# Kernel tuning notes

Hardware: AMD Instinct MI355X
Metric: run time of the kernel (lower is better)

Reference implementation:

```python
import jax, jax.numpy as jnp
import numpy as np

B, S, N = 1, 256, 384
MSA_S, Z_D = 64, 128
H, C_H = 8, 32
C_OPM = 32
INF = 1e9

def ln(x, w, b):
    mu = jnp.mean(x, -1, keepdims=True)
    var = jnp.mean(jnp.square(x - mu), -1, keepdims=True)
    return (x - mu) * jax.lax.rsqrt(var + 1e-5) * w + b

def setup_inputs() -> dict:
    key = jax.random.key(0)
    ks = jax.random.split(key, 16)
    def lin(k, out_d, in_d):
        return jax.random.normal(k, (out_d, in_d), jnp.float32) / np.sqrt(in_d)
    return {
        "z": jax.random.normal(ks[0], (B, N, N, Z_D), jnp.float32),
        "m": jax.random.normal(ks[1], (B, S, N, MSA_S), jnp.float32),
        "token_mask": jnp.ones((B, N, N), jnp.float32),
        "msa_mask": jnp.ones((B, S, N), jnp.float32),
        "norm_z_w": jnp.ones((Z_D,), jnp.float32), "norm_z_b": jnp.zeros((Z_D,), jnp.float32),
        "proj_z_w": lin(ks[2], H, Z_D),
        "norm_m_w": jnp.ones((MSA_S,), jnp.float32), "norm_m_b": jnp.zeros((MSA_S,), jnp.float32),
        "proj_m_w": lin(ks[3], H * C_H, MSA_S),
        "proj_g_w": lin(ks[4], H * C_H, MSA_S),
        "pwa_proj_o_w": lin(ks[5], MSA_S, H * C_H),
        "trans_norm_w": jnp.ones((MSA_S,), jnp.float32), "trans_norm_b": jnp.zeros((MSA_S,), jnp.float32),
        "fc1_w": lin(ks[6], 4 * MSA_S, MSA_S),
        "fc2_w": lin(ks[7], 4 * MSA_S, MSA_S),
        "fc3_w": lin(ks[8], MSA_S, 4 * MSA_S),
        "opm_norm_w": jnp.ones((MSA_S,), jnp.float32), "opm_norm_b": jnp.zeros((MSA_S,), jnp.float32),
        "proj_a_w": lin(ks[9], C_OPM, MSA_S),
        "proj_b_w": lin(ks[10], C_OPM, MSA_S),
        "opm_proj_o_w": lin(ks[11], Z_D, C_OPM * C_OPM),
        "opm_proj_o_b": jnp.zeros((Z_D,), jnp.float32),
    }

def reference(z, m, token_mask, msa_mask,
              norm_z_w, norm_z_b, proj_z_w,
              norm_m_w, norm_m_b, proj_m_w, proj_g_w, pwa_proj_o_w,
              trans_norm_w, trans_norm_b, fc1_w, fc2_w, fc3_w,
              opm_norm_w, opm_norm_b, proj_a_w, proj_b_w, opm_proj_o_w, opm_proj_o_b):
    # --- PairWeightedAveraging: pair-biased, gated MSA row attention ---
    b_full = ln(z, norm_z_w, norm_z_b) @ proj_z_w.T                     # [B,N,N,H]
    bias = jnp.transpose(b_full, (0, 3, 1, 2)) + (1.0 - token_mask[:, None]) * (-INF)
    w = jax.nn.softmax(bias, axis=-1)                                   # [B,H,N,N]
    mn = ln(m, norm_m_w, norm_m_b)
    v = (mn @ proj_m_w.T).reshape(B, S, N, H, C_H)                      # [B,S,N,H,c]
    g = jax.nn.sigmoid(mn @ proj_g_w.T)                                 # [B,S,N,H*c]
    o = jnp.einsum('bhij,bsjhd->bsihd', w, v).reshape(B, S, N, H * C_H)
    m = m + (g * o) @ pwa_proj_o_w.T
    # --- MSA transition (SwiGLU) ---
    tn = ln(m, trans_norm_w, trans_norm_b)
    m = m + (jax.nn.silu(tn @ fc1_w.T) * (tn @ fc2_w.T)) @ fc3_w.T
    # --- OuterProductMean -> pair update ---
    mk = msa_mask[..., None]                                            # [B,S,N,1]
    on = ln(m, opm_norm_w, opm_norm_b)
    a = (on @ proj_a_w.T) * mk                                          # [B,S,N,c]
    bb = (on @ proj_b_w.T) * mk                                         # [B,S,N,c]
    num_mask = jnp.clip(jnp.einsum('bsi,bsj->bij', msa_mask, msa_mask), 1.0, None)[..., None]
    opm = jnp.einsum('bsic,bsjd->bijcd', a, bb).reshape(B, N, N, C_OPM * C_OPM) / num_mask
    z = z + opm @ opm_proj_o_w.T + opm_proj_o_b
    return (z, m)
```

## Files before the change

### kernel.cpp

```cpp
#include <hip/hip_runtime.h>
#include <math.h>

constexpr int NRES = 384;
constexpr int NSEQ = 256;
constexpr int DM   = 64;
constexpr int DZ   = 128;
constexpr int NH   = 8;
constexpr int DH   = 32;
constexpr int HC   = NH * DH;
constexpr int DOP  = 32;
constexpr int FF   = 4 * DM;

constexpr int NPAIR = NRES * NRES;
constexpr int NROWS = NSEQ * NRES;
constexpr int ZTOT  = NPAIR * DZ;
constexpr int SD    = NSEQ * DH;

typedef unsigned short ushort_t;
typedef __attribute__((ext_vector_type(8))) short short8;
typedef __attribute__((ext_vector_type(4))) short short4_t;
typedef __attribute__((ext_vector_type(4))) float f32x4;

__device__ __forceinline__ float wred_sum(float v) {
    #pragma unroll
    for (int off = 32; off; off >>= 1) v += __shfl_xor(v, off, 64);
    return v;
}
__device__ __forceinline__ float sigm(float x) { return 1.0f / (1.0f + expf(-x)); }
__device__ __forceinline__ ushort_t cvt_bf(float f) {
    unsigned u = __float_as_uint(f);
    unsigned r = (u + 0x7FFFu + ((u >> 16) & 1u)) >> 16;
    return (ushort_t)r;
}
__device__ __forceinline__ float cvt_f(ushort_t h) {
    return __uint_as_float(((unsigned)h) << 16);
}
__device__ __forceinline__ f32x4 mfma16(short8 a, short8 b, f32x4 c) {
    return __builtin_amdgcn_mfma_f32_16x16x32_bf16(a, b, c, 0, 0, 0);
}
__device__ __forceinline__ void gld16(const ushort_t* g, ushort_t* l) {
    __builtin_amdgcn_global_load_lds(
        (const __attribute__((address_space(1))) unsigned int*)g,
        (__attribute__((address_space(3))) unsigned int*)l, 16, 0, 0);
}

__global__ __launch_bounds__(256) void k_prep(const float* __restrict__ f1,
                                              const float* __restrict__ f2,
                                              const float* __restrict__ f3,
                                              const float* __restrict__ opW,
                                              const float* __restrict__ pmw,
                                              const float* __restrict__ pgw,
                                              const float* __restrict__ pow_,
                                              const float* __restrict__ paw,
                                              const float* __restrict__ pbw,
                                              const float* __restrict__ pzw,
                                              ushort_t* __restrict__ f1b,
                                              ushort_t* __restrict__ f2b,
                                              ushort_t* __restrict__ f3b,
                                              ushort_t* __restrict__ opWb,
                                              ushort_t* __restrict__ pmwb,
                                              ushort_t* __restrict__ pgwb,
                                              ushort_t* __restrict__ powb,
                                              ushort_t* __restrict__ abwb,
                                              ushort_t* __restrict__ pzwb) {
    int i = blockIdx.x * 256 + threadIdx.x;
    opWb[i] = cvt_bf(opW[i]);
    if (i < FF * DM) {
        f1b[i] = cvt_bf(f1[i]);
        f2b[i] = cvt_bf(f2[i]);
        f3b[i] = cvt_bf(f3[i]);
    }
    if (i < HC * DM) {
        pmwb[i] = cvt_bf(pmw[i]);
        pgwb[i] = cvt_bf(pgw[i]);
        powb[i] = cvt_bf(pow_[i]);
    }
    if (i < 2 * DOP * DM) {
        abwb[i] = cvt_bf(i < DOP * DM ? paw[i] : pbw[i - DOP * DM]);
    }
    if (i < 16 * DZ) {
        pzwb[i] = (i < NH * DZ) ? cvt_bf(pzw[i]) : (ushort_t)0;
    }
}

__global__ __launch_bounds__(256) void k_biassm(const float* __restrict__ z,
                                                const float* __restrict__ nzw,
                                                const float* __restrict__ nzb,
                                                const ushort_t* __restrict__ pzwb,
                                                const float* __restrict__ tmask,
                                                ushort_t* __restrict__ wsb) {
    int i = blockIdx.x;
    __shared__ ushort_t Azl[128][136];
    __shared__ ushort_t Bl[16][136];
    __shared__ float ob[8][388];
    __shared__ float wln[128], bln[128];
    int t = threadIdx.x;
    if (t < 128) { wln[t] = nzw[t]; bln[t] = nzb[t]; }
    int wave = t >> 6, lane = t & 63;
    int lk = (lane >> 4) * 8, lr = lane & 15;
    int wr = wave * 32;
    for (int idx = t * 8; idx < 16 * DZ; idx += 256 * 8) {
        int row = idx >> 7, col = idx & 127;
        *(short8*)&Bl[row][col] = *(const short8*)&pzwb[idx];
    }
    __syncthreads();
    for (int c = 0; c < 3; c++) {
        {
            int jl = t >> 1, cb = (t & 1) * 64;
            const float* src = &z[((size_t)i * NRES + c * 128 + jl) * DZ + cb];
            float4 v[16];
            float s1 = 0.0f, s2 = 0.0f;
            #pragma unroll
            for (int q = 0; q < 16; q++) {
                v[q] = *(const float4*)&src[q * 4];
                s1 += v[q].x + v[q].y + v[q].z + v[q].w;
                s2 += v[q].x * v[q].x + v[q].y * v[q].y + v[q].z * v[q].z + v[q].w * v[q].w;
            }
            s1 += __shfl_xor(s1, 1, 64);
            s2 += __shfl_xor(s2, 1, 64);
            float mu = s1 * (1.0f / 128.0f);
            float var = s2 * (1.0f / 128.0f) - mu * mu;
            float rs = rsqrtf(var + 1e-5f);
            #pragma unroll
            for (int q = 0; q < 8; q++) {
                float4 xa = v[2 * q], xb = v[2 * q + 1];
                int base = cb + q * 8;
                short8 o;
                o[0] = (short)cvt_bf((xa.x - mu) * rs * wln[base + 0] + bln[base + 0]);
                o[1] = (short)cvt_bf((xa.y - mu) * rs * wln[base + 1] + bln[base + 1]);
                o[2] = (short)cvt_bf((xa.z - mu) * rs * wln[base + 2] + bln[base + 2]);
                o[3] = (short)cvt_bf((xa.w - mu) * rs * wln[base + 3] + bln[base + 3]);
                o[4] = (short)cvt_bf((xb.x - mu) * rs * wln[base + 4] + bln[base + 4]);
                o[5] = (short)cvt_bf((xb.y - mu) * rs * wln[base + 5] + bln[base + 5]);
                o[6] = (short)cvt_bf((xb.z - mu) * rs * wln[base + 6] + bln[base + 6]);
                o[7] = (short)cvt_bf((xb.w - mu) * rs * wln[base + 7] + bln[base + 7]);
                *(short8*)&Azl[jl][base] = o;
            }
        }
        __syncthreads();
        f32x4 acc[2] = {};
        #pragma unroll
        for (int ks = 0; ks < 4; ks++) {
            short8 b = *(const short8*)&Bl[lr][ks * 32 + lk];
            short8 a0 = *(const short8*)&Azl[wr + lr][ks * 32 + lk];
            short8 a1 = *(const short8*)&Azl[wr + 16 + lr][ks * 32 + lk];
            acc[0] = mfma16(a0, b, acc[0]);
            acc[1] = mfma16(a1, b, acc[1]);
        }
        if (lr < NH) {
            #pragma unroll
            for (int ri = 0; ri < 2; ri++) {
                int jb = c * 128 + wr + 16 * ri + (lane >> 4) * 4;
                #pragma unroll
                for (int r = 0; r < 4; r++)
                    ob[lr][jb + r] = acc[ri][r];
            }
        }
        __syncthreads();
    }
    int h = wave * 2 + (lane >> 5);
    int l32 = lane & 31;
    int jb = l32 * 12;
    const float* tm = &tmask[(size_t)i * NRES];
    float vals[12];
    float mx = -1e30f;
    #pragma unroll
    for (int q = 0; q < 12; q++) {
        float v = ob[h][jb + q] + (1.0f - tm[jb + q]) * (-1e9f);
        vals[q] = v;
        mx = fmaxf(mx, v);
    }
    #pragma unroll
    for (int off = 16; off; off >>= 1) mx = fmaxf(mx, __shfl_xor(mx, off, 64));
    float sum = 0.0f;
    #pragma unroll
    for (int q = 0; q < 12; q++) { vals[q] = expf(vals[q] - mx); sum += vals[q]; }
    #pragma unroll
    for (int off = 16; off; off >>= 1) sum += __shfl_xor(sum, off, 64);
    float inv = 1.0f / sum;
    ushort_t* o = &wsb[(size_t)h * NPAIR + (size_t)i * NRES + jb];
    #pragma unroll
    for (int q = 0; q < 12; q++) o[q] = cvt_bf(vals[q] * inv);
}

__global__ __launch_bounds__(256) void k_ln64(const float* __restrict__ src,
                                              const float* __restrict__ lw,
                                              const float* __restrict__ lb,
                                              ushort_t* __restrict__ dst) {
    int wave = threadIdx.x >> 6, lane = threadIdx.x & 63;
    int r = blockIdx.x * 4 + wave;
    float x = src[(size_t)r * DM + lane];
    float mu = wred_sum(x) * (1.0f / 64.0f);
    float d = x - mu;
    float var = wred_sum(d * d) * (1.0f / 64.0f);
    dst[(size_t)r * DM + lane] = cvt_bf(d * rsqrtf(var + 1e-5f) * lw[lane] + lb[lane]);
}

__global__ __launch_bounds__(256) void k_vproj_mfma(const ushort_t* __restrict__ A,
                                                    const ushort_t* __restrict__ Bt,
                                                    ushort_t* __restrict__ vtt) {
    int m0 = blockIdx.y * 64, n0c = blockIdx.x * 64;
    __shared__ ushort_t Al[64][40];
    __shared__ ushort_t Bl[64][40];
    __shared__ ushort_t ot[64][72];
    int t = threadIdx.x;
    int srow = t >> 2, sko = (t & 3) * 8;
    int wave = t >> 6, lane = t & 63;
    int wr = (wave >> 1) * 32, wc = (wave & 1) * 32;
    int lk = (lane >> 4) * 8, lr = lane & 15;
    f32x4 acc[2][2] = {};
    for (int k0 = 0; k0 < DM; k0 += 32) {
        *(short8*)&Al[srow][sko] = *(const short8*)&A[(size_t)(m0 + srow) * DM + k0 + sko];
        *(short8*)&Bl[srow][sko] = *(const short8*)&Bt[(size_t)(n0c + srow) * DM + k0 + sko];
        __syncthreads();
        short8 a0 = *(const short8*)&Al[wr + lr][lk];
        short8 a1 = *(const short8*)&Al[wr + 16 + lr][lk];
        short8 b0 = *(const short8*)&Bl[wc + lr][lk];
        short8 b1 = *(const short8*)&Bl[wc + 16 + lr][lk];
        acc[0][0] = mfma16(a0, b0, acc[0][0]);
        acc[0][1] = mfma16(a0, b1, acc[0][1]);
        acc[1][0] = mfma16(a1, b0, acc[1][0]);
        acc[1][1] = mfma16(a1, b1, acc[1][1]);
        __syncthreads();
    }
    #pragma unroll
    for (int ri = 0; ri < 2; ri++)
        #pragma unroll
        for (int ci = 0; ci < 2; ci++) {
            int rowb = wr + 16 * ri + (lane >> 4) * 4;
            int colb = wc + 16 * ci + lr;
            #pragma unroll
            for (int r = 0; r < 4; r++)
                ot[colb][rowb + r] = cvt_bf(acc[ri][ci][r]);
        }
    __syncthreads();
    int s = m0 / NRES, n0 = m0 % NRES;
    int h0 = n0c >> 5;
    int orow = t >> 2, seg = (t & 3) * 16;
    short8 v0 = *(const short8*)&ot[orow][seg];
    short8 v1 = *(const short8*)&ot[orow][seg + 8];
    int hh = orow >> 5, dd = orow & 31;
    ushort_t* dst = &vtt[(((size_t)(h0 + hh) * SD) + s * DH + dd) * NRES + n0 + seg];
    *(short8*)&dst[0] = v0;
    *(short8*)&dst[8] = v1;
}

__global__ __launch_bounds__(256) void k_tr(const ushort_t* __restrict__ src,
                                            ushort_t* __restrict__ dst,
                                            int R, int C) {
    size_t bs = (size_t)R * C;
    const ushort_t* s = src + blockIdx.z * bs;
    ushort_t* d = dst + blockIdx.z * bs;
    int r0 = blockIdx.y * 64, c0 = blockIdx.x * 64;
    __shared__ ushort_t tile[64][72];
    int t = threadIdx.x;
    int tr = t >> 2, tc = (t & 3) * 16;
    *(short8*)&tile[tr][tc]     = *(const short8*)&s[(size_t)(r0 + tr) * C + c0 + tc];
    *(short8*)&tile[tr][tc + 8] = *(const short8*)&s[(size_t)(r0 + tr) * C + c0 + tc + 8];
    __syncthreads();
    short8 o0, o1;
    #pragma unroll
    for (int i = 0; i < 8; i++) {
        o0[i] = (short)tile[tc + i][tr];
        o1[i] = (short)tile[tc + 8 + i][tr];
    }
    *(short8*)&d[(size_t)(c0 + tr) * R + r0 + tc]     = o0;
    *(short8*)&d[(size_t)(c0 + tr) * R + r0 + tc + 8] = o1;
}

__global__ __launch_bounds__(256) void k_attn_mfma(const ushort_t* __restrict__ wsb,
                                                   const ushort_t* __restrict__ vtt,
                                                   ushort_t* __restrict__ otb2) {
    int h = blockIdx.z;
    const ushort_t* A  = wsb + (size_t)h * NPAIR;
    const ushort_t* Bt = vtt + (size_t)h * SD * NRES;
    int m0 = blockIdx.y * 128, n0 = blockIdx.x * 128;
    __shared__ ushort_t Al[128 * 32];
    __shared__ ushort_t Bl[128 * 32];
    int t = threadIdx.x;
    int w = t >> 6, lane = t & 63;
    int wr = (w >> 1) * 64, wc = (w & 1) * 64;
    int lq = lane >> 4, lr = lane & 15;
    int rS = w * 16 + (lane >> 2);
    int cqs = (((lane & 3) ^ ((rS >> 1) & 3)) << 3);
    f32x4 acc[4][4] = {};
    for (int k0 = 0; k0 < NRES; k0 += 32) {
        gld16(&A [(size_t)(m0 + rS)      * NRES + k0 + cqs], &Al[(w * 16) * 32]);
        gld16(&A [(size_t)(m0 + 64 + rS) * NRES + k0 + cqs], &Al[(64 + w * 16) * 32]);
        gld16(&Bt[(size_t)(n0 + rS)      * NRES + k0 + cqs], &Bl[(w * 16) * 32]);
        gld16(&Bt[(size_t)(n0 + 64 + rS) * NRES + k0 + cqs], &Bl[(64 + w * 16) * 32]);
        __syncthreads();
        short8 af[4], bf2[4];
        #pragma unroll
        for (int i = 0; i < 4; i++) {
            int ra = wr + 16 * i + lr;
            int rb = wc + 16 * i + lr;
            af[i]  = *(const short8*)&Al[ra * 32 + ((lq ^ ((ra >> 1) & 3)) << 3)];
            bf2[i] = *(const short8*)&Bl[rb * 32 + ((lq ^ ((rb >> 1) & 3)) << 3)];
        }
        #pragma unroll
        for (int ri = 0; ri < 4; ri++)
            #pragma unroll
            for (int ci = 0; ci < 4; ci++)
                acc[ri][ci] = mfma16(af[ri], bf2[ci], acc[ri][ci]);
        __syncthreads();
    }
    #pragma unroll
    for (int ri = 0; ri < 4; ri++)
        #pragma unroll
        for (int ci = 0; ci < 4; ci++) {
            int row0 = m0 + wr + 16 * ri + (lane >> 4) * 4;
            int col  = n0 + wc + 16 * ci + lr;
            int s = col >> 5, dd = col & 31;
            #pragma unroll
            for (int r = 0; r < 4; r++)
                otb2[((size_t)s * NRES + row0 + r) * HC + h * DH + dd] = cvt_bf(acc[ri][ci][r]);
        }
}

__global__ __launch_bounds__(256) void k_gateout(const ushort_t* __restrict__ A,
                                                 const ushort_t* __restrict__ Bg,
                                                 const ushort_t* __restrict__ otb2,
                                                 const ushort_t* __restrict__ Bo,
                                                 const float* __restrict__ m,
                                                 float* __restrict__ mout,
                                                 const float* __restrict__ tnw,
                                                 const float* __restrict__ tnb,
                                                 ushort_t* __restrict__ tn_bf) {
    int m0 = blockIdx.x * 64;
    __shared__ ushort_t Al[64][72];
    __shared__ ushort_t Bl[64][72];
    __shared__ ushort_t go[64][264];
    int t = threadIdx.x;
    int srow = t >> 2, sko = (t & 3) * 16;
    int wave = t >> 6, lane = t & 63;
    int wr = (wave >> 1) * 32, wc = (wave & 1) * 32;
    int lk = (lane >> 4) * 8, lr = lane & 15;
    float tw = tnw[lane], tb = tnb[lane];
    {
        const ushort_t* arow = &A[(size_t)(m0 + srow) * DM + sko];
        *(short8*)&Al[srow][sko]     = *(const short8*)&arow[0];
        *(short8*)&Al[srow][sko + 8] = *(const short8*)&arow[8];
    }
    __syncthreads();
    short8 a[2][2];
    a[0][0] = *(const short8*)&Al[wr + lr][lk];
    a[0][1] = *(const short8*)&Al[wr + lr][32 + lk];
    a[1][0] = *(const short8*)&Al[wr + 16 + lr][lk];
    a[1][1] = *(const short8*)&Al[wr + 16 + lr][32 + lk];
    for (int nq = 0; nq < 4; nq++) {
        __syncthreads();
        {
            const ushort_t* brow = &Bg[(size_t)(nq * 64 + srow) * DM + sko];
            *(short8*)&Bl[srow][sko]     = *(const short8*)&brow[0];
            *(short8*)&Bl[srow][sko + 8] = *(const short8*)&brow[8];
        }
        __syncthreads();
        f32x4 acc[2][2] = {};
        #pragma unroll
        for (int ks = 0; ks < 2; ks++) {
            short8 b0 = *(const short8*)&Bl[wc + lr][ks * 32 + lk];
            short8 b1 = *(const short8*)&Bl[wc + 16 + lr][ks * 32 + lk];
            acc[0][0] = mfma16(a[0][ks], b0, acc[0][0]);
            acc[0][1] = mfma16(a[0][ks], b1, acc[0][1]);
            acc[1][0] = mfma16(a[1][ks], b0, acc[1][0]);
            acc[1][1] = mfma16(a[1][ks], b1, acc[1][1]);
        }
        #pragma unroll
        for (int ri = 0; ri < 2; ri++)
            #pragma unroll
            for (int ci = 0; ci < 2; ci++) {
                int lrow = wr + 16 * ri + (lane >> 4) * 4;
                int col  = nq * 64 + wc + 16 * ci + lr;
                #pragma unroll
                for (int r = 0; r < 4; r++) {
                    float ov = cvt_f(otb2[(size_t)(m0 + lrow + r) * HC + col]);
                    go[lrow + r][col] = cvt_bf(sigm(acc[ri][ci][r]) * ov);
                }
            }
    }
    f32x4 acc[2][2] = {};
    for (int k0 = 0; k0 < HC; k0 += 32) {
        __syncthreads();
        *(short8*)&Bl[t >> 2][(t & 3) * 8] = *(const short8*)&Bo[(size_t)(t >> 2) * HC + k0 + (t & 3) * 8];
        __syncthreads();
        short8 a0 = *(const short8*)&go[wr + lr][k0 + lk];
        short8 a1 = *(const short8*)&go[wr + 16 + lr][k0 + lk];
        short8 b0 = *(const short8*)&Bl[wc + lr][lk];
        short8 b1 = *(const short8*)&Bl[wc + 16 + lr][lk];
        acc[0][0] = mfma16(a0, b0, acc[0][0]);
        acc[0][1] = mfma16(a0, b1, acc[0][1]);
        acc[1][0] = mfma16(a1, b0, acc[1][0]);
        acc[1][1] = mfma16(a1, b1, acc[1][1]);
    }
    __syncthreads();
    #pragma unroll
    for (int ri = 0; ri < 2; ri++)
        #pragma unroll
        for (int ci = 0; ci < 2; ci++) {
            int lrow0 = wr + 16 * ri + (lane >> 4) * 4;
            int col   = wc + 16 * ci + lr;
            #pragma unroll
            for (int r = 0; r < 4; r++) {
                size_t idx = (size_t)(m0 + lrow0 + r) * DM + col;
                float v = m[idx] + acc[ri][ci][r];
                mout[idx] = v;
                go[lrow0 + r][col] = cvt_bf(v);
            }
        }
    __syncthreads();
    for (int rr = 0; rr < 16; rr++) {
        int row = wave * 16 + rr;
        float x = cvt_f(go[row][lane]);
        float mu = wred_sum(x) * (1.0f / 64.0f);
        float d = x - mu;
        float var = wred_sum(d * d) * (1.0f / 64.0f);
        tn_bf[(size_t)(m0 + row) * DM + lane] = cvt_bf(d * rsqrtf(var + 1e-5f) * tw + tb);
    }
}

__global__ __launch_bounds__(256) void k_fctrans(const ushort_t* __restrict__ A,
                                                 const ushort_t* __restrict__ B1,
                                                 const ushort_t* __restrict__ B2,
                                                 const ushort_t* __restrict__ B3,
                                                 float* __restrict__ mio,
                                                 const float* __restrict__ onw,
                                                 const float* __restrict__ onb,
                                                 ushort_t* __restrict__ onb_bf) {
    int m0 = blockIdx.x * 64;
    __shared__ ushort_t Al[64][72];
    __shared__ ushort_t B1l[64][72];
    __shared__ ushort_t B2l[64][72];
    __shared__ ushort_t hhl[64][264];
    int t = threadIdx.x;
    int srow = t >> 2, sko = (t & 3) * 16;
    int wave = t >> 6, lane = t & 63;
    int wr = (wave >> 1) * 32, wc = (wave & 1) * 32;
    int lk = (lane >> 4) * 8, lr = lane & 15;
    float ow = onw[lane], ob = onb[lane];
    {
        const ushort_t* arow = &A[(size_t)(m0 + srow) * DM + sko];
        *(short8*)&Al[srow][sko]     = *(const short8*)&arow[0];
        *(short8*)&Al[srow][sko + 8] = *(const short8*)&arow[8];
    }
    __syncthreads();
    short8 a[2][2];
    a[0][0] = *(const short8*)&Al[wr + lr][lk];
    a[0][1] = *(const short8*)&Al[wr + lr][32 + lk];
    a[1][0] = *(const short8*)&Al[wr + 16 + lr][lk];
    a[1][1] = *(const short8*)&Al[wr + 16 + lr][32 + lk];
    for (int nq = 0; nq < 4; nq++) {
        __syncthreads();
        {
            const ushort_t* b1r = &B1[(size_t)(nq * 64 + srow) * DM + sko];
            const ushort_t* b2r = &B2[(size_t)(nq * 64 + srow) * DM + sko];
            *(short8*)&B1l[srow][sko]     = *(const short8*)&b1r[0];
            *(short8*)&B1l[srow][sko + 8] = *(const short8*)&b1r[8];
            *(short8*)&B2l[srow][sko]     = *(const short8*)&b2r[0];
            *(short8*)&B2l[srow][sko + 8] = *(const short8*)&b2r[8];
        }
        __syncthreads();
        f32x4 acc1[2][2] = {}, acc2[2][2] = {};
        #pragma unroll
        for (int ks = 0; ks < 2; ks++) {
            short8 p0 = *(const short8*)&B1l[wc + lr][ks * 32 + lk];
            short8 p1 = *(const short8*)&B1l[wc + 16 + lr][ks * 32 + lk];
            short8 q0 = *(const short8*)&B2l[wc + lr][ks * 32 + lk];
            short8 q1 = *(const short8*)&B2l[wc + 16 + lr][ks * 32 + lk];
            acc1[0][0] = mfma16(a[0][ks], p0, acc1[0][0]);
            acc1[0][1] = mfma16(a[0][ks], p1, acc1[0][1]);
            acc1[1][0] = mfma16(a[1][ks], p0, acc1[1][0]);
            acc1[1][1] = mfma16(a[1][ks], p1, acc1[1][1]);
            acc2[0][0] = mfma16(a[0][ks], q0, acc2[0][0]);
            acc2[0][1] = mfma16(a[0][ks], q1, acc2[0][1]);
            acc2[1][0] = mfma16(a[1][ks], q0, acc2[1][0]);
            acc2[1][1] = mfma16(a[1][ks], q1, acc2[1][1]);
        }
        #pragma unroll
        for (int ri = 0; ri < 2; ri++)
            #pragma unroll
            for (int ci = 0; ci < 2; ci++) {
                int lrow = wr + 16 * ri + (lane >> 4) * 4;
                int col  = nq * 64 + wc + 16 * ci + lr;
                #pragma unroll
                for (int r = 0; r < 4; r++) {
                    float a1v = acc1[ri][ci][r], a2v = acc2[ri][ci][r];
                    hhl[lrow + r][col] = cvt_bf(a1v * sigm(a1v) * a2v);
                }
            }
    }
    f32x4 acc[2][2] = {};
    for (int k0 = 0; k0 < FF; k0 += 32) {
        __syncthreads();
        *(short8*)&B1l[t >> 2][(t & 3) * 8] = *(const short8*)&B3[(size_t)(t >> 2) * FF + k0 + (t & 3) * 8];
        __syncthreads();
        short8 a0 = *(const short8*)&hhl[wr + lr][k0 + lk];
        short8 a1 = *(const short8*)&hhl[wr + 16 + lr][k0 + lk];
        short8 b0 = *(const short8*)&B1l[wc + lr][lk];
        short8 b1 = *(const short8*)&B1l[wc + 16 + lr][lk];
        acc[0][0] = mfma16(a0, b0, acc[0][0]);
        acc[0][1] = mfma16(a0, b1, acc[0][1]);
        acc[1][0] = mfma16(a1, b0, acc[1][0]);
        acc[1][1] = mfma16(a1, b1, acc[1][1]);
    }
    __syncthreads();
    #pragma unroll
    for (int ri = 0; ri < 2; ri++)
        #pragma unroll
        for (int ci = 0; ci < 2; ci++) {
            int lrow0 = wr + 16 * ri + (lane >> 4) * 4;
            int col   = wc + 16 * ci + lr;
            #pragma unroll
            for (int r = 0; r < 4; r++) {
                size_t idx = (size_t)(m0 + lrow0 + r) * DM + col;
                float v = mio[idx] + acc[ri][ci][r];
                mio[idx] = v;
                hhl[lrow0 + r][col] = cvt_bf(v);
            }
        }
    __syncthreads();
    for (int rr = 0; rr < 16; rr++) {
        int row = wave * 16 + rr;
        float x = cvt_f(hhl[row][lane]);
        float mu = wred_sum(x) * (1.0f / 64.0f);
        float d = x - mu;
        float var = wred_sum(d * d) * (1.0f / 64.0f);
        onb_bf[(size_t)(m0 + row) * DM + lane] = cvt_bf(d * rsqrtf(var + 1e-5f) * ow + ob);
    }
}

__global__ __launch_bounds__(256) void k_ab_mfma(const ushort_t* __restrict__ A,
                                                 const ushort_t* __restrict__ Bt,
                                                 const float* __restrict__ smask,
                                                 ushort_t* __restrict__ abuf,
                                                 ushort_t* __restrict__ bbuf) {
    int m0 = blockIdx.x * 64;
    __shared__ ushort_t Al[64][40];
    __shared__ ushort_t Bl[64][40];
    int t = threadIdx.x;
    int srow = t >> 2, sko = (t & 3) * 8;
    int wave = t >> 6, lane = t & 63;
    int wr = (wave >> 1) * 32, wc = (wave & 1) * 32;
    int lk = (lane >> 4) * 8, lr = lane & 15;
    f32x4 acc[2][2] = {};
    for (int k0 = 0; k0 < DM; k0 += 32) {
        *(short8*)&Al[srow][sko] = *(const short8*)&A[(size_t)(m0 + srow) * DM + k0 + sko];
        *(short8*)&Bl[srow][sko] = *(const short8*)&Bt[(size_t)srow * DM + k0 + sko];
        __syncthreads();
        short8 a0 = *(const short8*)&Al[wr + lr][lk];
        short8 a1 = *(const short8*)&Al[wr + 16 + lr][lk];
        short8 b0 = *(const short8*)&Bl[wc + lr][lk];
        short8 b1 = *(const short8*)&Bl[wc + 16 + lr][lk];
        acc[0][0] = mfma16(a0, b0, acc[0][0]);
        acc[0][1] = mfma16(a0, b1, acc[0][1]);
        acc[1][0] = mfma16(a1, b0, acc[1][0]);
        acc[1][1] = mfma16(a1, b1, acc[1][1]);
        __syncthreads();
    }
    #pragma unroll
    for (int ri = 0; ri < 2; ri++)
        #pragma unroll
        for (int ci = 0; ci < 2; ci++) {
            int row0 = m0 + wr + 16 * ri + (lane >> 4) * 4;
            int col  = wc + 16 * ci + lr;
            #pragma unroll
            for (int r = 0; r < 4; r++) {
                int rr = row0 + r;
                int s = rr / NRES, n = rr % NRES;
                float v = acc[ri][ci][r] * smask[rr];
                if (col < DOP)
                    abuf[(size_t)s * (NRES * DOP) + n * DOP + col] = cvt_bf(v);
                else
                    bbuf[(size_t)s * (NRES * DOP) + n * DOP + (col - DOP)] = cvt_bf(v);
            }
        }
}

__global__ __launch_bounds__(256) void k_msum(const float* __restrict__ smask,
                                              float* __restrict__ msum) {
    int i0 = blockIdx.y * 64, j0 = blockIdx.x * 64;
    __shared__ float As[16][64];
    __shared__ float Bs[16][64];
    int t = threadIdx.x;
    int ty = t >> 4, tx = t & 15;
    float acc[4][4] = {};
    for (int k0 = 0; k0 < NSEQ; k0 += 16) {
        int kk = t >> 4, x4 = (t & 15) * 4;
        *(float4*)&As[kk][x4] = *(const float4*)&smask[(size_t)(k0 + kk) * NRES + i0 + x4];
        *(float4*)&Bs[kk][x4] = *(const float4*)&smask[(size_t)(k0 + kk) * NRES + j0 + x4];
        __syncthreads();
        #pragma unroll
        for (int k = 0; k < 16; k++) {
            float4 a4 = *(const float4*)&As[k][ty * 4];
            float4 b4 = *(const float4*)&Bs[k][tx * 4];
            float ar[4] = {a4.x, a4.y, a4.z, a4.w};
            float br[4] = {b4.x, b4.y, b4.z, b4.w};
            #pragma unroll
            for (int i2 = 0; i2 < 4; i2++)
                #pragma unroll
                for (int j2 = 0; j2 < 4; j2++)
                    acc[i2][j2] += ar[i2] * br[j2];
        }
        __syncthreads();
    }
    #pragma unroll
    for (int r = 0; r < 4; r++) {
        float4 o4 = make_float4(fmaxf(acc[r][0], 1.0f), fmaxf(acc[r][1], 1.0f),
                                fmaxf(acc[r][2], 1.0f), fmaxf(acc[r][3], 1.0f));
        *(float4*)&msum[(size_t)(i0 + ty * 4 + r) * NRES + j0 + tx * 4] = o4;
    }
}

__global__ __launch_bounds__(256) void k_opm_mfma(const ushort_t* __restrict__ At,
                                                  const ushort_t* __restrict__ Bt,
                                                  ushort_t* __restrict__ opmc) {
    int m0 = blockIdx.y * 128;
    int n0 = blockIdx.x * 128;
    __shared__ ushort_t Al[128 * 32];
    __shared__ ushort_t Bl[128 * 32];
    int t = threadIdx.x;
    int w = t >> 6, lane = t & 63;
    int wr = (w >> 1) * 64, wc = (w & 1) * 64;
    int lq = lane >> 4, lr = lane & 15;
    int rS = w * 16 + (lane >> 2);
    int cqs = (((lane & 3) ^ ((rS >> 1) & 3)) << 3);
    f32x4 acc[4][4] = {};
    for (int k0 = 0; k0 < NSEQ; k0 += 32) {
        gld16(&At[(size_t)(m0 + rS)      * NSEQ + k0 + cqs], &Al[(w * 16) * 32]);
        gld16(&At[(size_t)(m0 + 64 + rS) * NSEQ + k0 + cqs], &Al[(64 + w * 16) * 32]);
        gld16(&Bt[(size_t)(n0 + rS)      * NSEQ + k0 + cqs], &Bl[(w * 16) * 32]);
        gld16(&Bt[(size_t)(n0 + 64 + rS) * NSEQ + k0 + cqs], &Bl[(64 + w * 16) * 32]);
        __syncthreads();
        short8 af[4], bf2[4];
        #pragma unroll
        for (int i = 0; i < 4; i++) {
            int ra = wr + 16 * i + lr;
            int rb = wc + 16 * i + lr;
            af[i]  = *(const short8*)&Al[ra * 32 + ((lq ^ ((ra >> 1) & 3)) << 3)];
            bf2[i] = *(const short8*)&Bl[rb * 32 + ((lq ^ ((rb >> 1) & 3)) << 3)];
        }
        #pragma unroll
        for (int ri = 0; ri < 4; ri++)
            #pragma unroll
            for (int ci = 0; ci < 4; ci++)
                acc[ri][ci] = mfma16(bf2[ci], af[ri], acc[ri][ci]);
        __syncthreads();
    }
    #pragma unroll
    for (int ri = 0; ri < 4; ri++)
        #pragma unroll
        for (int ci = 0; ci < 4; ci++) {
            int ml = m0 + wr + 16 * ri + lr;
            int il = ml >> 5, c = ml & 31;
            int nl = n0 + wc + 16 * ci + lq * 4;
            int j = nl >> 5, dd = nl & 31;
            short4_t pk;
            #pragma unroll
            for (int r = 0; r < 4; r++) pk[r] = (short)cvt_bf(acc[ri][ci][r]);
            *(short4_t*)&opmc[((size_t)(il * NRES + j) << 10) + (c << 5) + dd] = pk;
        }
}

__global__ __launch_bounds__(256) void k_proj_mfma(const ushort_t* __restrict__ A,
                                                   const ushort_t* __restrict__ Bt,
                                                   const float* __restrict__ opB,
                                                   const float* __restrict__ msum,
                                                   const float* __restrict__ zin,
                                                   float* __restrict__ zout,
                                                   int ib) {
    int m0 = blockIdx.x * 128;
    __shared__ ushort_t Al[128 * 32];
    __shared__ ushort_t Bl[128 * 32];
    int t = threadIdx.x;
    int w = t >> 6, lane = t & 63;
    int wr = (w >> 1) * 64, wc = (w & 1) * 64;
    int lq = lane >> 4, lr = lane & 15;
    int rS = w * 16 + (lane >> 2);
    int cqs = (((lane & 3) ^ ((rS >> 1) & 3)) << 3);
    f32x4 acc[4][4] = {};
    for (int k0 = 0; k0 < 1024; k0 += 32) {
        gld16(&A [(size_t)(m0 + rS)      * 1024 + k0 + cqs], &Al[(w * 16) * 32]);
        gld16(&A [(size_t)(m0 + 64 + rS) * 1024 + k0 + cqs], &Al[(64 + w * 16) * 32]);
        gld16(&Bt[(size_t)(rS)           * 1024 + k0 + cqs], &Bl[(w * 16) * 32]);
        gld16(&Bt[(size_t)(64 + rS)      * 1024 + k0 + cqs], &Bl[(64 + w * 16) * 32]);
        __syncthreads();
        short8 af[4], bf2[4];
        #pragma unroll
        for (int i = 0; i < 4; i++) {
            int ra = wr + 16 * i + lr;
            int rb = wc + 16 * i + lr;
            af[i]  = *(const short8*)&Al[ra * 32 + ((lq ^ ((ra >> 1) & 3)) << 3)];
            bf2[i] = *(const short8*)&Bl[rb * 32 + ((lq ^ ((rb >> 1) & 3)) << 3)];
        }
        #pragma unroll
        for (int ri = 0; ri < 4; ri++)
            #pragma unroll
            for (int ci = 0; ci < 4; ci++)
                acc[ri][ci] = mfma16(af[ri], bf2[ci], acc[ri][ci]);
        __syncthreads();
    }
    #pragma unroll
    for (int ri = 0; ri < 4; ri++)
        #pragma unroll
        for (int ci = 0; ci < 4; ci++) {
            int row0 = m0 + wr + 16 * ri + (lane >> 4) * 4;
            int col  = wc + 16 * ci + lr;
            #pragma unroll
            for (int r = 0; r < 4; r++) {
                size_t G = (size_t)ib * NRES + row0 + r;
                float inv = 1.0f / msum[G];
                zout[G * DZ + col] = zin[G * DZ + col] + acc[ri][ci][r] * inv + opB[col];
            }
        }
}

extern "C" void kernel_launch(void* const* d_in, const int* in_sizes, int n_in,
                              void* d_out, int out_size, void* d_ws, size_t ws_size,
                              hipStream_t stream) {
    const float* z     = (const float*)d_in[0];
    const float* m     = (const float*)d_in[1];
    const float* tmask = (const float*)d_in[2];
    const float* smask = (const float*)d_in[3];
    const float* nzw   = (const float*)d_in[4];
    const float* nzb   = (const float*)d_in[5];
    const float* pzw   = (const float*)d_in[6];
    const float* nmw   = (const float*)d_in[7];
    const float* nmb   = (const float*)d_in[8];
    const float* pmw   = (const float*)d_in[9];
    const float* pgw   = (const float*)d_in[10];
    const float* pow_  = (const float*)d_in[11];
    const float* tnw   = (const float*)d_in[12];
    const float* tnb_  = (const float*)d_in[13];
    const float* f1    = (const float*)d_in[14];
    const float* f2    = (const float*)d_in[15];
    const float* f3    = (const float*)d_in[16];
    const float* onw   = (const float*)d_in[17];
    const float* onb   = (const float*)d_in[18];
    const float* paw   = (const float*)d_in[19];
    const float* pbw   = (const float*)d_in[20];
    const float* opW   = (const float*)d_in[21];
    const float* opB   = (const float*)d_in[22];

    float* zout = (float*)d_out;
    float* mout = zout + ZTOT;

    char* W = (char*)d_ws;
    ushort_t* wsb  = (ushort_t*)(W + 4718592);
    ushort_t* mnb  = (ushort_t*)(W + 7077888);
    ushort_t* vtt  = (ushort_t*)(W + 69992448);
    ushort_t* otb2 = (ushort_t*)(W + 120324096);
    ushort_t* tn_bf  = vtt;
    ushort_t* onb_bf = mnb;
    ushort_t* abuf = (ushort_t*)(W + 69992448 + 12582912);
    ushort_t* bbuf = (ushort_t*)(W + 69992448 + 18874368);

    bool big = ws_size >= 348200000ull;
    int ichunk, nchunks;
    ushort_t *opmc, *abt, *bbt;
    float* msum;
    ushort_t *f1b, *f2b, *f3b, *opWb, *pmwb, *pgwb, *powb, *abwb, *pzwb;
    if (big) {
        ichunk = NRES; nchunks = 1;
        opmc = (ushort_t*)(W + 19660800);
        abt  = (ushort_t*)(W + 321650688);
        bbt  = (ushort_t*)(W + 327942144);
        msum = (float*)(W + 346816512);
        f1b  = (ushort_t*)(W + 347406336);
        f2b  = (ushort_t*)(W + 347439104);
        f3b  = (ushort_t*)(W + 347471872);
        opWb = (ushort_t*)(W + 347504640);
        pmwb = (ushort_t*)(W + 347766784);
        pgwb = (ushort_t*)(W + 347799552);
        powb = (ushort_t*)(W + 347832320);
        abwb = (ushort_t*)(W + 347865088);
        pzwb = (ushort_t*)(W + 347873280);
    } else {
        ichunk = 96; nchunks = 4;
        opmc = (ushort_t*)(W + 19660800);
        abt  = otb2;
        bbt  = (ushort_t*)(W + 120324096 + 6291456);
        msum = (float*)(W + 170655744);
        f1b  = (ushort_t*)(W + 171245568);
        f2b  = (ushort_t*)(W + 171278336);
        f3b  = (ushort_t*)(W + 171311104);
        opWb = (ushort_t*)(W + 171343872);
        pmwb = (ushort_t*)(W + 171606016);
        pgwb = (ushort_t*)(W + 171638784);
        powb = (ushort_t*)(W + 171671552);
        abwb = (ushort_t*)(W + 171704320);
        pzwb = (ushort_t*)(W + 171712512);
    }

    k_prep<<<512, 256, 0, stream>>>(f1, f2, f3, opW, pmw, pgw, pow_, paw, pbw, pzw,
                                    f1b, f2b, f3b, opWb, pmwb, pgwb, powb, abwb, pzwb);

    k_biassm<<<NRES, 256, 0, stream>>>(z, nzw, nzb, pzwb, tmask, wsb);
    k_ln64<<<NROWS / 4, 256, 0, stream>>>(m, nmw, nmb, mnb);
    k_vproj_mfma<<<dim3(HC / 64, NROWS / 64), 256, 0, stream>>>(mnb, pmwb, vtt);
    k_attn_mfma<<<dim3(SD / 128, NRES / 128, NH), 256, 0, stream>>>(wsb, vtt, otb2);
    k_gateout<<<NROWS / 64, 256, 0, stream>>>(mnb, pgwb, otb2, powb, m, mout, tnw, tnb_, tn_bf);

    k_fctrans<<<NROWS / 64, 256, 0, stream>>>(tn_bf, f1b, f2b, f3b, mout, onw, onb, onb_bf);

    k_ab_mfma<<<NROWS / 64, 256, 0, stream>>>(onb_bf, abwb, smask, abuf, bbuf);
    k_tr<<<dim3((NRES * DOP) / 64, NSEQ / 64, 2), 256, 0, stream>>>(abuf, abt, NSEQ, NRES * DOP);
    k_msum<<<dim3(NRES / 64, NRES / 64), 256, 0, stream>>>(smask, msum);
    for (int cb = 0; cb < nchunks; cb++) {
        int ib = cb * ichunk;
        const ushort_t* Achunk = abt + (size_t)(ib * DOP) * NSEQ;
        k_opm_mfma<<<dim3((NRES * DOP) / 128, (ichunk * DOP) / 128), 256, 0, stream>>>(Achunk, bbt, opmc);
        k_proj_mfma<<<(ichunk * NRES) / 128, 256, 0, stream>>>(opmc, opWb, opB, msum, z, zout, ib);
    }
}
```

Baseline: 485.6 us.

## Store OPM intermediate and output projection weights in FP8 and use FP8 MFMA

The outer-product intermediate (N*N*1024 values) and the opm projection weights are now quantized to FP8 instead of bf16, halving the bytes written and read for the largest intermediate. The projection GEMM switches to the fp8 16x16x32 MFMA with a simplified LDS load layout. The epilogue is also restructured to use float4 loads and stores of z and the bias. FP8 quantization of unscaled OPM sums risks precision loss or overflow beyond tolerance.

```diff
diff --git a/kernel.cpp b/kernel.cpp
--- a/kernel.cpp
+++ b/kernel.cpp
@@ -17,6 +17,8 @@
 constexpr int SD    = NSEQ * DH;
 
 typedef unsigned short ushort_t;
+typedef unsigned char uchar_t;
+typedef long long i64;
 typedef __attribute__((ext_vector_type(8))) short short8;
 typedef __attribute__((ext_vector_type(4))) short short4_t;
 typedef __attribute__((ext_vector_type(4))) float f32x4;
@@ -38,7 +40,10 @@
 __device__ __forceinline__ f32x4 mfma16(short8 a, short8 b, f32x4 c) {
     return __builtin_amdgcn_mfma_f32_16x16x32_bf16(a, b, c, 0, 0, 0);
 }
-__device__ __forceinline__ void gld16(const ushort_t* g, ushort_t* l) {
+__device__ __forceinline__ f32x4 mfma16f8(i64 a, i64 b, f32x4 c) {
+    return __builtin_amdgcn_mfma_f32_16x16x32_fp8_fp8(a, b, c, 0, 0, 0);
+}
+__device__ __forceinline__ void gld16(const void* g, void* l) {
     __builtin_amdgcn_global_load_lds(
         (const __attribute__((address_space(1))) unsigned int*)g,
         (__attribute__((address_space(3))) unsigned int*)l, 16, 0, 0);
@@ -57,14 +62,14 @@
                                               ushort_t* __restrict__ f1b,
                                               ushort_t* __restrict__ f2b,
                                               ushort_t* __restrict__ f3b,
-                                              ushort_t* __restrict__ opWb,
+                                              uchar_t* __restrict__ opW8,
                                               ushort_t* __restrict__ pmwb,
                                               ushort_t* __restrict__ pgwb,
                                               ushort_t* __restrict__ powb,
                                               ushort_t* __restrict__ abwb,
                                               ushort_t* __restrict__ pzwb) {
     int i = blockIdx.x * 256 + threadIdx.x;
-    opWb[i] = cvt_bf(opW[i]);
+    opW8[i] = (uchar_t)(__builtin_amdgcn_cvt_pk_fp8_f32(opW[i], 0.0f, 0, 0) & 0xff);
     if (i < FF * DM) {
         f1b[i] = cvt_bf(f1[i]);
         f2b[i] = cvt_bf(f2[i]);
@@ -613,7 +618,7 @@
 
 __global__ __launch_bounds__(256) void k_opm_mfma(const ushort_t* __restrict__ At,
                                                   const ushort_t* __restrict__ Bt,
-                                                  ushort_t* __restrict__ opmc) {
+                                                  uchar_t* __restrict__ opmc8) {
     int m0 = blockIdx.y * 128;
     int n0 = blockIdx.x * 128;
     __shared__ ushort_t Al[128 * 32];
@@ -654,64 +659,63 @@
             int il = ml >> 5, c = ml & 31;
             int nl = n0 + wc + 16 * ci + lq * 4;
             int j = nl >> 5, dd = nl & 31;
-            short4_t pk;
-            #pragma unroll
-            for (int r = 0; r < 4; r++) pk[r] = (short)cvt_bf(acc[ri][ci][r]);
-            *(short4_t*)&opmc[((size_t)(il * NRES + j) << 10) + (c << 5) + dd] = pk;
-        }
-}
-
-__global__ __launch_bounds__(256) void k_proj_mfma(const ushort_t* __restrict__ A,
-                                                   const ushort_t* __restrict__ Bt,
+            int p01  = __builtin_amdgcn_cvt_pk_fp8_f32(acc[ri][ci][0], acc[ri][ci][1], 0, 0);
+            int pall = __builtin_amdgcn_cvt_pk_fp8_f32(acc[ri][ci][2], acc[ri][ci][3], p01, 1);
+            *(int*)&opmc8[((size_t)(il * NRES + j) << 10) + (c << 5) + dd] = pall;
+        }
+}
+
+__global__ __launch_bounds__(256) void k_proj_mfma(const uchar_t* __restrict__ A,
+                                                   const uchar_t* __restrict__ Bt,
                                                    const float* __restrict__ opB,
                                                    const float* __restrict__ msum,
                                                    const float* __restrict__ zin,
                                                    float* __restrict__ zout,
                                                    int ib) {
     int m0 = blockIdx.x * 128;
-    __shared__ ushort_t Al[128 * 32];
-    __shared__ ushort_t Bl[128 * 32];
+    __shared__ uchar_t Al[128 * 32];
+    __shared__ uchar_t Bl[128 * 32];
     int t = threadIdx.x;
     int w = t >> 6, lane = t & 63;
     int wr = (w >> 1) * 64, wc = (w & 1) * 64;
     int lq = lane >> 4, lr = lane & 15;
-    int rS = w * 16 + (lane >> 2);
-    int cqs = (((lane & 3) ^ ((rS >> 1) & 3)) << 3);
+    int rS = lane >> 1, cS = (lane & 1) * 16;
     f32x4 acc[4][4] = {};
     for (int k0 = 0; k0 < 1024; k0 += 32) {
-        gld16(&A [(size_t)(m0 + rS)      * 1024 + k0 + cqs], &Al[(w * 16) * 32]);
-        gld16(&A [(size_t)(m0 + 64 + rS) * 1024 + k0 + cqs], &Al[(64 + w * 16) * 32]);
-        gld16(&Bt[(size_t)(rS)           * 1024 + k0 + cqs], &Bl[(w * 16) * 32]);
-        gld16(&Bt[(size_t)(64 + rS)      * 1024 + k0 + cqs], &Bl[(64 + w * 16) * 32]);
-        __syncthreads();
-        short8 af[4], bf2[4];
+        gld16(&A [(size_t)(m0 + w * 32 + rS) * 1024 + k0 + cS], &Al[(w * 32) * 32]);
+        gld16(&Bt[(size_t)(w * 32 + rS)      * 1024 + k0 + cS], &Bl[(w * 32) * 32]);
+        __syncthreads();
+        i64 af[4], bf2[4];
         #pragma unroll
         for (int i = 0; i < 4; i++) {
-            int ra = wr + 16 * i + lr;
-            int rb = wc + 16 * i + lr;
-            af[i]  = *(const short8*)&Al[ra * 32 + ((lq ^ ((ra >> 1) & 3)) << 3)];
-            bf2[i] = *(const short8*)&Bl[rb * 32 + ((lq ^ ((rb >> 1) & 3)) << 3)];
+            af[i]  = *(const i64*)&Al[(wr + 16 * i + lr) * 32 + lq * 8];
+            bf2[i] = *(const i64*)&Bl[(wc + 16 * i + lr) * 32 + lq * 8];
         }
         #pragma unroll
         for (int ri = 0; ri < 4; ri++)
             #pragma unroll
             for (int ci = 0; ci < 4; ci++)
-                acc[ri][ci] = mfma16(af[ri], bf2[ci], acc[ri][ci]);
-        __syncthreads();
-    }
-    #pragma unroll
-    for (int ri = 0; ri < 4; ri++)
+                acc[ri][ci] = mfma16f8(bf2[ci], af[ri], acc[ri][ci]);
+        __syncthreads();
+    }
+    #pragma unroll
+    for (int ri = 0; ri < 4; ri++) {
+        int p = m0 + wr + 16 * ri + lr;
+        size_t G = (size_t)ib * NRES + p;
+        float inv = 1.0f / msum[G];
         #pragma unroll
         for (int ci = 0; ci < 4; ci++) {
-            int row0 = m0 + wr + 16 * ri + (lane >> 4) * 4;
-            int col  = wc + 16 * ci + lr;
-            #pragma unroll
-            for (int r = 0; r < 4; r++) {
-                size_t G = (size_t)ib * NRES + row0 + r;
-                float inv = 1.0f / msum[G];
-                zout[G * DZ + col] = zin[G * DZ + col] + acc[ri][ci][r] * inv + opB[col];
-            }
-        }
+            int e0 = wc + 16 * ci + lq * 4;
+            float4 zv = *(const float4*)&zin[G * DZ + e0];
+            float4 bv = *(const float4*)&opB[e0];
+            float4 o4;
+            o4.x = zv.x + acc[ri][ci][0] * inv + bv.x;
+            o4.y = zv.y + acc[ri][ci][1] * inv + bv.y;
+            o4.z = zv.z + acc[ri][ci][2] * inv + bv.z;
+            o4.w = zv.w + acc[ri][ci][3] * inv + bv.w;
+            *(float4*)&zout[G * DZ + e0] = o4;
+        }
+    }
 }
 
 extern "C" void kernel_launch(void* const* d_in, const int* in_sizes, int n_in,
@@ -756,19 +760,20 @@
 
     bool big = ws_size >= 348200000ull;
     int ichunk, nchunks;
-    ushort_t *opmc, *abt, *bbt;
+    uchar_t *opmc8, *opW8;
+    ushort_t *abt, *bbt;
     float* msum;
-    ushort_t *f1b, *f2b, *f3b, *opWb, *pmwb, *pgwb, *powb, *abwb, *pzwb;
+    ushort_t *f1b, *f2b, *f3b, *pmwb, *pgwb, *powb, *abwb, *pzwb;
     if (big) {
         ichunk = NRES; nchunks = 1;
-        opmc = (ushort_t*)(W + 19660800);
+        opmc8 = (uchar_t*)(W + 19660800);
         abt  = (ushort_t*)(W + 321650688);
         bbt  = (ushort_t*)(W + 327942144);
         msum = (float*)(W + 346816512);
         f1b  = (ushort_t*)(W + 347406336);
         f2b  = (ushort_t*)(W + 347439104);
         f3b  = (ushort_t*)(W + 347471872);
-        opWb = (ushort_t*)(W + 347504640);
+        opW8 = (uchar_t*)(W + 347504640);
         pmwb = (ushort_t*)(W + 347766784);
         pgwb = (ushort_t*)(W + 347799552);
         powb = (ushort_t*)(W + 347832320);
@@ -776,14 +781,14 @@
         pzwb = (ushort_t*)(W + 347873280);
     } else {
         ichunk = 96; nchunks = 4;
-        opmc = (ushort_t*)(W + 19660800);
+        opmc8 = (uchar_t*)(W + 19660800);
         abt  = otb2;
         bbt  = (ushort_t*)(W + 120324096 + 6291456);
         msum = (float*)(W + 170655744);
         f1b  = (ushort_t*)(W + 171245568);
         f2b  = (ushort_t*)(W + 171278336);
         f3b  = (ushort_t*)(W + 171311104);
-        opWb = (ushort_t*)(W + 171343872);
+        opW8 = (uchar_t*)(W + 171343872);
         pmwb = (ushort_t*)(W + 171606016);
         pgwb = (ushort_t*)(W + 171638784);
         powb = (ushort_t*)(W + 171671552);
@@ -792,7 +797,7 @@
     }
 
     k_prep<<<512, 256, 0, stream>>>(f1, f2, f3, opW, pmw, pgw, pow_, paw, pbw, pzw,
-                                    f1b, f2b, f3b, opWb, pmwb, pgwb, powb, abwb, pzwb);
+                                    f1b, f2b, f3b, opW8, pmwb, pgwb, powb, abwb, pzwb);
 
     k_biassm<<<NRES, 256, 0, stream>>>(z, nzw, nzb, pzwb, tmask, wsb);
     k_ln64<<<NROWS / 4, 256, 0, stream>>>(m, nmw, nmb, mnb);
@@ -808,7 +813,7 @@
     for (int cb = 0; cb < nchunks; cb++) {
         int ib = cb * ichunk;
         const ushort_t* Achunk = abt + (size_t)(ib * DOP) * NSEQ;
-        k_opm_mfma<<<dim3((NRES * DOP) / 128, (ichunk * DOP) / 128), 256, 0, stream>>>(Achunk, bbt, opmc);
-        k_proj_mfma<<<(ichunk * NRES) / 128, 256, 0, stream>>>(opmc, opWb, opB, msum, z, zout, ib);
-    }
-}
+        k_opm_mfma<<<dim3((NRES * DOP) / 128, (ichunk * DOP) / 128), 256, 0, stream>>>(Achunk, bbt, opmc8);
+        k_proj_mfma<<<(ichunk * NRES) / 128, 256, 0, stream>>>(opmc8, opW8, opB, msum, z, zout, ib);
+    }
+}
```

New measurement: 478.6 us. No clear change (-1.5%).
